# Optimization experiments

Measured on AMD Instinct MI355X. Metric: run time of the kernel, lower is better.

Reference implementation:

```python
import jax, jax.numpy as jnp
import numpy as np
from jax import lax

B, C, TX, TY = 16, 192, 512, 2048
SEG = 8192 // 256  # segment_frames = 32 (hop length 256)
NEG_INF = -1e9


def setup_inputs() -> dict:
    key = jax.random.key(0)
    ks = jax.random.split(key, 7)
    z = jax.random.normal(ks[0], (B, C, TY), jnp.float32)
    z_p = jax.random.normal(ks[1], (B, C, TY), jnp.float32)
    m_p = jax.random.normal(ks[2], (B, C, TX), jnp.float32)
    logs_p = 0.1 * jax.random.normal(ks[3], (B, C, TX), jnp.float32)
    x_lengths = jax.random.randint(ks[4], (B,), TX // 2, TX + 1, jnp.int32)
    y_lengths = jax.random.randint(ks[5], (B,), TY // 2, TY + 1, jnp.int32)
    rand_u = jax.random.uniform(ks[6], (B,), jnp.float32)
    return dict(z=z, z_p=z_p, m_p=m_p, logs_p=logs_p,
                x_lengths=x_lengths, y_lengths=y_lengths, rand_u=rand_u)


def neg_cent_fn(z_p, m_p, logs_p):
    # sum_c -0.5 * exp(-2 logs)[c,tx] * (z_p[c,ty] - m_p[c,tx])^2 - sum_c logs[c,tx]
    # expanded (z-m)^2 = z^2 - 2 z m + m^2 -> batched GEMMs (same math as broadcast form)
    s = jnp.exp(-2.0 * logs_p)                                 # [B,C,Tx]
    a = jnp.einsum('bct,bcs->bts', -0.5 * z_p * z_p, s)        # [B,Ty,Tx]
    b = jnp.einsum('bct,bcs->bts', z_p, s * m_p)               # [B,Ty,Tx]
    c = jnp.sum(-0.5 * s * m_p * m_p - logs_p, axis=1)         # [B,Tx]
    return a + b + c[:, None, :]


def maximum_path_single(value, t_x, t_y):
    # Monotonic alignment search DP on value [Ty,Tx], valid region [:t_y,:t_x].
    Ty, Tx = value.shape
    tx = jnp.arange(Tx)

    def fwd(v, row):
        v_shift = jnp.concatenate([jnp.full((1,), NEG_INF, v.dtype), v[:-1]])
        dirn = v_shift > v                      # True: best predecessor is tx-1
        v_new = row + jnp.maximum(v, v_shift)
        v_new = jnp.where(tx < t_x, v_new, NEG_INF)
        v_new = jnp.maximum(v_new, NEG_INF)     # clamp accumulation
        return v_new, dirn

    v0 = jnp.where(tx == 0, 0.0, NEG_INF)
    _, dirs = lax.scan(fwd, v0, value)          # dirs [Ty,Tx] bool

    def bwd(idx, j):
        active = j < t_y
        idx = jnp.where(j == t_y - 1, t_x - 1, idx)
        row = jnp.where(active, jnp.zeros((Tx,), value.dtype).at[idx].set(1.0), 0.0)
        idx = jnp.where(active, idx - dirs[j, idx].astype(idx.dtype), idx)
        return idx, row

    _, path_rev = lax.scan(bwd, jnp.int32(0), jnp.arange(Ty - 1, -1, -1))
    return path_rev[::-1]                       # [Ty,Tx] 0/1 path


def rand_slice_segments(z, y_lengths, rand_u):
    t = z.shape[2]
    safe = jnp.minimum(y_lengths, t)
    ids_max = jnp.maximum(safe - SEG, 0)
    ids = (rand_u * (ids_max.astype(jnp.float32) + 1e-8)).astype(jnp.int32)
    zs = jax.vmap(lambda zi, s: lax.dynamic_slice_in_dim(zi, s, SEG, axis=1))(z, ids)
    valid = (jnp.arange(SEG)[None, None, :] < (safe - ids)[:, None, None])
    return zs * valid.astype(z.dtype), ids


def reference(z, z_p, m_p, logs_p, x_lengths, y_lengths, rand_u):
    neg_cent = neg_cent_fn(z_p, m_p, logs_p)                     # [B,Ty,Tx]
    attn = jax.vmap(maximum_path_single)(neg_cent, x_lengths, y_lengths)
    attn = lax.stop_gradient(attn)                               # torch: no_grad + detach
    m_p_a = jnp.einsum('bts,bcs->bct', attn, m_p)                # [B,C,Ty]
    logs_p_a = jnp.einsum('bts,bcs->bct', attn, logs_p)          # [B,C,Ty]
    z_slice, ids_slice = rand_slice_segments(z, y_lengths, rand_u)
    return z_slice, ids_slice, attn, m_p_a, logs_p_a
```

## Files before the change

kernel.cpp:

```cpp
#include <hip/hip_runtime.h>
#include <stdint.h>

#define B_   16
#define C_   192
#define TX_  512
#define TY_  2048
#define K_   384
#define SEG_ 32
#define NEG_INF_ (-1e9f)


__global__ __launch_bounds__(128) void k_prep(const float* __restrict__ mp,
                                              const float* __restrict__ logsp,
                                              float* __restrict__ Bmat,
                                              float* __restrict__ cterm) {
    int b  = blockIdx.y;
    int tx = blockIdx.x * 128 + threadIdx.x;
    const float* mb = mp    + (size_t)b * C_ * TX_ + tx;
    const float* lb = logsp + (size_t)b * C_ * TX_ + tx;
    float* B0 = Bmat + (size_t)b * K_ * TX_ + tx;
    float acc = 0.f;
    for (int c = 0; c < C_; ++c) {
        float lg = lb[(size_t)c * TX_];
        float m  = mb[(size_t)c * TX_];
        float s  = expf(-2.f * lg);
        B0[(size_t)c * TX_]        = s;
        B0[(size_t)(C_ + c) * TX_] = s * m;
        acc += -0.5f * s * m * m - lg;
    }
    cterm[b * TX_ + tx] = acc;
}

__global__ __launch_bounds__(256) void k_gemm(const float* __restrict__ zp,
                                              const float* __restrict__ Bmat,
                                              const float* __restrict__ cterm,
                                              float* __restrict__ ncout) {
    __shared__ float As[16][128];
    __shared__ float Bs[16][128];
    int b  = blockIdx.z;
    int m0 = blockIdx.y * 128;
    int n0 = blockIdx.x * 128;
    int tid = threadIdx.x;
    int tm = tid >> 4;
    int tn = tid & 15;
    const float* zpb = zp   + (size_t)b * C_ * TY_;
    const float* Bb  = Bmat + (size_t)b * K_ * TX_;

    float acc[8][8];
#pragma unroll
    for (int i = 0; i < 8; ++i)
#pragma unroll
        for (int j = 0; j < 8; ++j) acc[i][j] = 0.f;

    int lrow = tid >> 5;
    int lcol = (tid & 31) << 2;

    for (int k0 = 0; k0 < K_; k0 += 16) {
        int ksrc = (k0 < C_) ? k0 : (k0 - C_);
        const float* Ab = zpb + (size_t)(ksrc + lrow) * TY_ + m0 + lcol;
        float4 z0 = *(const float4*)Ab;
        float4 z1 = *(const float4*)(Ab + (size_t)8 * TY_);
        if (k0 < C_) {
            z0.x = -0.5f * z0.x * z0.x; z0.y = -0.5f * z0.y * z0.y;
            z0.z = -0.5f * z0.z * z0.z; z0.w = -0.5f * z0.w * z0.w;
            z1.x = -0.5f * z1.x * z1.x; z1.y = -0.5f * z1.y * z1.y;
            z1.z = -0.5f * z1.z * z1.z; z1.w = -0.5f * z1.w * z1.w;
        }
        const float* Bp = Bb + (size_t)(k0 + lrow) * TX_ + n0 + lcol;
        float4 w0 = *(const float4*)Bp;
        float4 w1 = *(const float4*)(Bp + (size_t)8 * TX_);

        __syncthreads();
        *(float4*)&As[lrow][lcol]     = z0;
        *(float4*)&As[lrow + 8][lcol] = z1;
        *(float4*)&Bs[lrow][lcol]     = w0;
        *(float4*)&Bs[lrow + 8][lcol] = w1;
        __syncthreads();

#pragma unroll
        for (int kk = 0; kk < 16; ++kk) {
            float4 a0 = *(const float4*)&As[kk][tm * 8];
            float4 a1 = *(const float4*)&As[kk][tm * 8 + 4];
            float4 b0 = *(const float4*)&Bs[kk][tn * 8];
            float4 b1 = *(const float4*)&Bs[kk][tn * 8 + 4];
            float a[8]  = {a0.x, a0.y, a0.z, a0.w, a1.x, a1.y, a1.z, a1.w};
            float bb[8] = {b0.x, b0.y, b0.z, b0.w, b1.x, b1.y, b1.z, b1.w};
#pragma unroll
            for (int i = 0; i < 8; ++i)
#pragma unroll
                for (int j = 0; j < 8; ++j)
                    acc[i][j] = fmaf(a[i], bb[j], acc[i][j]);
        }
    }

    float cadd[8];
#pragma unroll
    for (int j = 0; j < 8; ++j) cadd[j] = cterm[b * TX_ + n0 + tn * 8 + j];

#pragma unroll
    for (int i = 0; i < 8; ++i) {
        int row = m0 + tm * 8 + i;
        float* orow = ncout + ((size_t)b * TY_ + row) * TX_ + n0 + tn * 8;
        float4 o0, o1;
        o0.x = acc[i][0] + cadd[0]; o0.y = acc[i][1] + cadd[1];
        o0.z = acc[i][2] + cadd[2]; o0.w = acc[i][3] + cadd[3];
        o1.x = acc[i][4] + cadd[4]; o1.y = acc[i][5] + cadd[5];
        o1.z = acc[i][6] + cadd[6]; o1.w = acc[i][7] + cadd[7];
        *(float4*)orow       = o0;
        *(float4*)(orow + 4) = o1;
    }
}

#define NSLOT_ 3

__global__ __launch_bounds__(256, 1) void k_dp(const float* __restrict__ nc,
                                               const int* __restrict__ xl,
                                               const int* __restrict__ yl,
                                               int* __restrict__ path) {
    extern __shared__ unsigned char sdirs[];
    unsigned* sdirs32 = (unsigned*)sdirs;
    float*    stagef  = (float*)(sdirs + 131072);
    unsigned* flags   = (unsigned*)(sdirs + 131072 + NSLOT_ * 8192);
    unsigned* cons_ctr = flags + NSLOT_;

    int b    = blockIdx.x;
    int tid  = threadIdx.x;
    int w    = tid >> 6;
    int lane = tid & 63;
    int t_x  = xl[b];
    int t_y  = yl[b]; if (t_y > TY_) t_y = TY_;
    const float* ncb = nc + (size_t)b * TY_ * TX_;
    int ng = (t_y + 3) >> 2;

    if (tid < NSLOT_ + 1) flags[tid] = 0;
    __syncthreads();

    if (w != 0) {
        int cv = (int)__hip_atomic_load(cons_ctr, __ATOMIC_ACQUIRE,
                                        __HIP_MEMORY_SCOPE_WORKGROUP);
        for (int g = w - 1; g < ng; g += 3) {
            while (cv < g - 2) {
                __builtin_amdgcn_s_sleep(1);
                cv = (int)__hip_atomic_load(cons_ctr, __ATOMIC_ACQUIRE,
                                            __HIP_MEMORY_SCOPE_WORKGROUP);
            }
            int j0 = g * 4;
            float* sb = stagef + (g % NSLOT_) * 2048;
#pragma unroll
            for (int r = 0; r < 4; ++r) {
                const float4* row = (const float4*)(ncb + (size_t)(j0 + r) * TX_);
                float4 q0 = row[2 * lane];
                float4 q1 = row[2 * lane + 1];
                *(float4*)(sb + r * 512 + lane * 4)       = q0;
                *(float4*)(sb + r * 512 + 256 + lane * 4) = q1;
            }
            if (lane == 0)
                __hip_atomic_store(&flags[g % NSLOT_], (unsigned)(g + 1),
                                   __ATOMIC_RELEASE, __HIP_MEMORY_SCOPE_WORKGROUP);
            cv = (int)__hip_atomic_load(cons_ctr, __ATOMIC_ACQUIRE,
                                        __HIP_MEMORY_SCOPE_WORKGROUP);
        }
        return;
    }

    int col0 = lane * 8;
    float v[8];
#pragma unroll
    for (int k = 0; k < 8; ++k) v[k] = (col0 + k == 0) ? 0.f : NEG_INF_;

    const unsigned neg_bits = __float_as_uint(NEG_INF_);
    unsigned fv = 0;
    for (int g = 0; g < ng; ++g) {
        while (fv != (unsigned)(g + 1))
            fv = __hip_atomic_load(&flags[g % NSLOT_], __ATOMIC_ACQUIRE,
                                   __HIP_MEMORY_SCOPE_WORKGROUP);
        unsigned fnx = __hip_atomic_load(&flags[(g + 1) % NSLOT_], __ATOMIC_ACQUIRE,
                                         __HIP_MEMORY_SCOPE_WORKGROUP);
        const float* rowp = stagef + (g % NSLOT_) * 2048;
        unsigned dw = 0u;
#pragma unroll
        for (int r = 0; r < 4; ++r) {
            float4 p0 = *(const float4*)(rowp + r * 512 + lane * 4);
            float4 p1 = *(const float4*)(rowp + r * 512 + 256 + lane * 4);
            float rc[8] = {p0.x, p0.y, p0.z, p0.w, p1.x, p1.y, p1.z, p1.w};
            float left = __uint_as_float(__builtin_amdgcn_update_dpp(
                (int)neg_bits, (int)__float_as_uint(v[7]),
                0x138 , 0xF, 0xF, false));
            unsigned by = 0u;
#pragma unroll
            for (int k = 7; k >= 0; --k) {
                float vs = (k == 0) ? left : v[k - 1];
                if (vs > v[k]) by |= (1u << k);
                v[k] = fmaxf(v[k], vs) + rc[k];
            }
            dw |= by << (8 * r);
        }
        sdirs32[g * 64 + lane] = dw;
        if (lane == 0)
            __hip_atomic_store(cons_ctr, (unsigned)(g + 1),
                               __ATOMIC_RELEASE, __HIP_MEMORY_SCOPE_WORKGROUP);
        fv = fnx;
    }

    int* pb = path + b * TY_;
    for (int j = t_y + lane; j < TY_; j += 64) pb[j] = -1;

    if (lane == 0) {
        int idx = t_x - 1;
        int j   = t_y - 1;
        while (j >= 0) {
            int n  = (j + 1 < 8) ? (j + 1) : 8;
            int bs = (idx - 7) >> 3; if (bs < 0) bs = 0;
            int b2 = bs + 1;         if (b2 > 63) b2 = 63;
            unsigned lo[8], hi[8];
#pragma unroll
            for (int r = 0; r < 8; ++r) {
                if (r < n) {
                    int jr = j - r;
                    int rb = (jr >> 2) * 256 + (jr & 3);
                    lo[r] = sdirs[rb + bs * 4];
                    hi[r] = sdirs[rb + b2 * 4];
                }
            }
#pragma unroll
            for (int r = 0; r < 8; ++r) {
                if (r < n) {
                    pb[j - r] = idx;
                    int Bi = idx >> 3;
                    unsigned byte = (Bi == bs) ? lo[r] : hi[r];
                    idx -= (int)((byte >> (idx & 7)) & 1u);
                }
            }
            j -= n;
        }
    }
}

__global__ __launch_bounds__(256) void k_attn(const int* __restrict__ path,
                                              float* __restrict__ attn) {
    int i   = blockIdx.x * 256 + threadIdx.x;
    int tx0 = (i & 127) << 2;
    int bty = i >> 7;
    int p   = path[bty];
    float4 o;
    o.x = (p == tx0)     ? 1.f : 0.f;
    o.y = (p == tx0 + 1) ? 1.f : 0.f;
    o.z = (p == tx0 + 2) ? 1.f : 0.f;
    o.w = (p == tx0 + 3) ? 1.f : 0.f;
    ((float4*)attn)[i] = o;
}

__global__ __launch_bounds__(256) void k_proj(const int* __restrict__ path,
                                              const float* __restrict__ mp,
                                              const float* __restrict__ logsp,
                                              float* __restrict__ mpa,
                                              float* __restrict__ logsa) {
    int i   = blockIdx.x * 256 + threadIdx.x;
    int ty0 = (i & 511) << 2;
    int bc  = i >> 9;
    int b   = bc / C_;
    const int4 p4 = *(const int4*)(path + b * TY_ + ty0);
    const float* mrow = mp    + (size_t)bc * TX_;
    const float* lrow = logsp + (size_t)bc * TX_;
    float4 mo, lo;
    mo.x = (p4.x >= 0) ? mrow[p4.x] : 0.f;  lo.x = (p4.x >= 0) ? lrow[p4.x] : 0.f;
    mo.y = (p4.y >= 0) ? mrow[p4.y] : 0.f;  lo.y = (p4.y >= 0) ? lrow[p4.y] : 0.f;
    mo.z = (p4.z >= 0) ? mrow[p4.z] : 0.f;  lo.z = (p4.z >= 0) ? lrow[p4.z] : 0.f;
    mo.w = (p4.w >= 0) ? mrow[p4.w] : 0.f;  lo.w = (p4.w >= 0) ? lrow[p4.w] : 0.f;
    ((float4*)mpa)[i]   = mo;
    ((float4*)logsa)[i] = lo;
}

__global__ __launch_bounds__(256) void k_slice(const float* __restrict__ z,
                                               const int* __restrict__ yl,
                                               const float* __restrict__ ru,
                                               float* __restrict__ zs,
                                               float* __restrict__ oid) {
    int b = blockIdx.x;
    int safe = yl[b]; if (safe > TY_) safe = TY_;
    int idsmax = safe - SEG_; if (idsmax < 0) idsmax = 0;
    int ids = (int)(ru[b] * ((float)idsmax + 1e-8f));
    int lim = safe - ids;
    for (int t = threadIdx.x; t < C_ * SEG_; t += 256) {
        int c = t >> 5, k = t & 31;
        zs[b * C_ * SEG_ + t] =
            (k < lim) ? z[((size_t)b * C_ + c) * TY_ + ids + k] : 0.f;
    }
    if (threadIdx.x == 0) oid[b] = (float)ids;
}

extern "C" void kernel_launch(void* const* d_in, const int* in_sizes, int n_in,
                              void* d_out, int out_size, void* d_ws, size_t ws_size,
                              hipStream_t stream) {
    const float* z     = (const float*)d_in[0];
    const float* zp    = (const float*)d_in[1];
    const float* mp    = (const float*)d_in[2];
    const float* logsp = (const float*)d_in[3];
    const int*   xl    = (const int*)d_in[4];
    const int*   yl    = (const int*)d_in[5];
    const float* ru    = (const float*)d_in[6];

    float* out     = (float*)d_out;
    float* o_zs    = out;
    float* o_ids   = out + 98304;
    float* o_attn  = out + 98320;
    float* o_mpa   = out + 16875536;
    float* o_logsa = out + 23166992;

    float* Bmat  = (float*)d_ws;
    float* cterm = Bmat + (size_t)B_ * K_ * TX_;
    int*   path  = (int*)(cterm + B_ * TX_);

    const int dp_lds = 131072 + NSLOT_ * 8192 + 64;

    hipFuncSetAttribute((const void*)k_dp,
                        hipFuncAttributeMaxDynamicSharedMemorySize, dp_lds);

    hipLaunchKernelGGL(k_prep, dim3(TX_ / 128, B_), dim3(128), 0, stream,
                       mp, logsp, Bmat, cterm);
    hipLaunchKernelGGL(k_gemm, dim3(TX_ / 128, TY_ / 128, B_), dim3(256), 0, stream,
                       zp, Bmat, cterm, o_attn);
    hipLaunchKernelGGL(k_dp, dim3(B_), dim3(256), dp_lds, stream,
                       o_attn, xl, yl, path);
    hipLaunchKernelGGL(k_attn, dim3(B_ * TY_ * TX_ / 4 / 256), dim3(256), 0, stream,
                       path, o_attn);
    hipLaunchKernelGGL(k_proj, dim3(B_ * C_ * TY_ / 4 / 256), dim3(256), 0, stream,
                       path, mp, logsp, o_mpa, o_logsa);
    hipLaunchKernelGGL(k_slice, dim3(B_), dim3(256), 0, stream,
                       z, yl, ru, o_zs, o_ids);
}
```

Measured before the change: 843.4 us.

## Deepen DP producer pipeline and spill direction bits to global memory

The DP kernel now runs 512 threads with 7 producer waves and a 14-slot LDS staging ring, where before it had 3 producers and 3 slots. The goal is to keep the serial forward wavefront from stalling on loads of neg_cent rows. To free LDS for the larger ring, direction bytes go to a global workspace instead of LDS. The backtrack now stages 64-row windows cooperatively from global into LDS before lane 0 walks them. This adds global write and read traffic and a waitcnt fence, and relies on workspace space that was not allocated before.

```diff
diff --git a/kernel.cpp b/kernel.cpp
--- a/kernel.cpp
+++ b/kernel.cpp
@@ -111,17 +111,18 @@
     }
 }
 
-#define NSLOT_ 3
-
-__global__ __launch_bounds__(256, 1) void k_dp(const float* __restrict__ nc,
+#define NS_ 14
+#define NP_ 7
+
+__global__ __launch_bounds__(512, 1) void k_dp(const float* __restrict__ nc,
                                                const int* __restrict__ xl,
                                                const int* __restrict__ yl,
-                                               int* __restrict__ path) {
-    extern __shared__ unsigned char sdirs[];
-    unsigned* sdirs32 = (unsigned*)sdirs;
-    float*    stagef  = (float*)(sdirs + 131072);
-    unsigned* flags   = (unsigned*)(sdirs + 131072 + NSLOT_ * 8192);
-    unsigned* cons_ctr = flags + NSLOT_;
+                                               int* __restrict__ path,
+                                               unsigned char* __restrict__ gdirs) {
+    extern __shared__ unsigned char slds[];
+    float*    stagef   = (float*)slds;
+    unsigned* flags    = (unsigned*)(slds + NS_ * 8192);
+    unsigned* cons_ctr = flags + NS_;
 
     int b    = blockIdx.x;
     int tid  = threadIdx.x;
@@ -130,22 +131,23 @@
     int t_x  = xl[b];
     int t_y  = yl[b]; if (t_y > TY_) t_y = TY_;
     const float* ncb = nc + (size_t)b * TY_ * TX_;
+    unsigned char* gb = gdirs + (size_t)b * (TY_ * 64);
     int ng = (t_y + 3) >> 2;
 
-    if (tid < NSLOT_ + 1) flags[tid] = 0;
+    if (tid < NS_ + 1) flags[tid] = 0u;
     __syncthreads();
 
     if (w != 0) {
         int cv = (int)__hip_atomic_load(cons_ctr, __ATOMIC_ACQUIRE,
                                         __HIP_MEMORY_SCOPE_WORKGROUP);
-        for (int g = w - 1; g < ng; g += 3) {
-            while (cv < g - 2) {
+        for (int g = w - 1; g < ng; g += NP_) {
+            while (cv < g - (NS_ - 1)) {
                 __builtin_amdgcn_s_sleep(1);
                 cv = (int)__hip_atomic_load(cons_ctr, __ATOMIC_ACQUIRE,
                                             __HIP_MEMORY_SCOPE_WORKGROUP);
             }
             int j0 = g * 4;
-            float* sb = stagef + (g % NSLOT_) * 2048;
+            float* sb = stagef + (g % NS_) * 2048;
 #pragma unroll
             for (int r = 0; r < 4; ++r) {
                 const float4* row = (const float4*)(ncb + (size_t)(j0 + r) * TX_);
@@ -155,7 +157,7 @@
                 *(float4*)(sb + r * 512 + 256 + lane * 4) = q1;
             }
             if (lane == 0)
-                __hip_atomic_store(&flags[g % NSLOT_], (unsigned)(g + 1),
+                __hip_atomic_store(&flags[g % NS_], (unsigned)(g + 1),
                                    __ATOMIC_RELEASE, __HIP_MEMORY_SCOPE_WORKGROUP);
             cv = (int)__hip_atomic_load(cons_ctr, __ATOMIC_ACQUIRE,
                                         __HIP_MEMORY_SCOPE_WORKGROUP);
@@ -172,11 +174,11 @@
     unsigned fv = 0;
     for (int g = 0; g < ng; ++g) {
         while (fv != (unsigned)(g + 1))
-            fv = __hip_atomic_load(&flags[g % NSLOT_], __ATOMIC_ACQUIRE,
+            fv = __hip_atomic_load(&flags[g % NS_], __ATOMIC_ACQUIRE,
                                    __HIP_MEMORY_SCOPE_WORKGROUP);
-        unsigned fnx = __hip_atomic_load(&flags[(g + 1) % NSLOT_], __ATOMIC_ACQUIRE,
+        unsigned fnx = __hip_atomic_load(&flags[(g + 1) % NS_], __ATOMIC_ACQUIRE,
                                          __HIP_MEMORY_SCOPE_WORKGROUP);
-        const float* rowp = stagef + (g % NSLOT_) * 2048;
+        const float* rowp = stagef + (g % NS_) * 2048;
         unsigned dw = 0u;
 #pragma unroll
         for (int r = 0; r < 4; ++r) {
@@ -195,44 +197,59 @@
             }
             dw |= by << (8 * r);
         }
-        sdirs32[g * 64 + lane] = dw;
+        int j0 = g * 4;
+        gb[(size_t)(j0    ) * 64 + lane] = (unsigned char)(dw      );
+        gb[(size_t)(j0 + 1) * 64 + lane] = (unsigned char)(dw >>  8);
+        gb[(size_t)(j0 + 2) * 64 + lane] = (unsigned char)(dw >> 16);
+        gb[(size_t)(j0 + 3) * 64 + lane] = (unsigned char)(dw >> 24);
         if (lane == 0)
             __hip_atomic_store(cons_ctr, (unsigned)(g + 1),
                                __ATOMIC_RELEASE, __HIP_MEMORY_SCOPE_WORKGROUP);
         fv = fnx;
     }
 
+    __builtin_amdgcn_s_waitcnt(3952);
+
     int* pb = path + b * TY_;
-    for (int j = t_y + lane; j < TY_; j += 64) pb[j] = -1;
-
-    if (lane == 0) {
-        int idx = t_x - 1;
-        int j   = t_y - 1;
-        while (j >= 0) {
-            int n  = (j + 1 < 8) ? (j + 1) : 8;
-            int bs = (idx - 7) >> 3; if (bs < 0) bs = 0;
-            int b2 = bs + 1;         if (b2 > 63) b2 = 63;
-            unsigned lo[8], hi[8];
-#pragma unroll
-            for (int r = 0; r < 8; ++r) {
-                if (r < n) {
-                    int jr = j - r;
-                    int rb = (jr >> 2) * 256 + (jr & 3);
-                    lo[r] = sdirs[rb + bs * 4];
-                    hi[r] = sdirs[rb + b2 * 4];
+    for (int j2 = t_y + lane; j2 < TY_; j2 += 64) pb[j2] = -1;
+
+    unsigned char* swin = (unsigned char*)stagef;
+    int j   = t_y - 1;
+    int idx = t_x - 1;
+    while (j >= 0) {
+        int nb = (j + 1 < 64) ? (j + 1) : 64;
+        if (lane < nb) {
+            const uint4* rp = (const uint4*)(gb + (size_t)(j - lane) * 64);
+            uint4 a0 = rp[0], a1 = rp[1], a2 = rp[2], a3 = rp[3];
+            uint4* wp = (uint4*)(swin + lane * 64);
+            wp[0] = a0; wp[1] = a1; wp[2] = a2; wp[3] = a3;
+        }
+        if (lane == 0) {
+            int r2 = 0;
+            while (r2 < nb) {
+                int n = nb - r2; if (n > 8) n = 8;
+                int Bhi = idx >> 3;
+                int Blo = Bhi - 1; if (Blo < 0) Blo = 0;
+                unsigned lo8[8], hi8[8];
+#pragma unroll
+                for (int r = 0; r < 8; ++r) {
+                    if (r < n) {
+                        lo8[r] = swin[(r2 + r) * 64 + Blo];
+                        hi8[r] = swin[(r2 + r) * 64 + Bhi];
+                    }
                 }
+#pragma unroll
+                for (int r = 0; r < 8; ++r) {
+                    if (r < n) {
+                        pb[j - (r2 + r)] = idx;
+                        unsigned byte = ((idx >> 3) == Bhi) ? hi8[r] : lo8[r];
+                        idx -= (int)((byte >> (idx & 7)) & 1u);
+                    }
+                }
+                r2 += n;
             }
-#pragma unroll
-            for (int r = 0; r < 8; ++r) {
-                if (r < n) {
-                    pb[j - r] = idx;
-                    int Bi = idx >> 3;
-                    unsigned byte = (Bi == bs) ? lo[r] : hi[r];
-                    idx -= (int)((byte >> (idx & 7)) & 1u);
-                }
-            }
-            j -= n;
-        }
+        }
+        j -= nb;
     }
 }
 
@@ -307,11 +324,12 @@
     float* o_mpa   = out + 16875536;
     float* o_logsa = out + 23166992;
 
-    float* Bmat  = (float*)d_ws;
-    float* cterm = Bmat + (size_t)B_ * K_ * TX_;
-    int*   path  = (int*)(cterm + B_ * TX_);
-
-    const int dp_lds = 131072 + NSLOT_ * 8192 + 64;
+    float*         Bmat  = (float*)d_ws;
+    float*         cterm = Bmat + (size_t)B_ * K_ * TX_;
+    int*           path  = (int*)(cterm + B_ * TX_);
+    unsigned char* gdirs = (unsigned char*)(path + B_ * TY_);
+
+    const int dp_lds = NS_ * 8192 + 64;
 
     hipFuncSetAttribute((const void*)k_dp,
                         hipFuncAttributeMaxDynamicSharedMemorySize, dp_lds);
@@ -320,8 +338,8 @@
                        mp, logsp, Bmat, cterm);
     hipLaunchKernelGGL(k_gemm, dim3(TX_ / 128, TY_ / 128, B_), dim3(256), 0, stream,
                        zp, Bmat, cterm, o_attn);
-    hipLaunchKernelGGL(k_dp, dim3(B_), dim3(256), dp_lds, stream,
-                       o_attn, xl, yl, path);
+    hipLaunchKernelGGL(k_dp, dim3(B_), dim3(512), dp_lds, stream,
+                       o_attn, xl, yl, path, gdirs);
     hipLaunchKernelGGL(k_attn, dim3(B_ * TY_ * TX_ / 4 / 256), dim3(256), 0, stream,
                        path, o_attn);
     hipLaunchKernelGGL(k_proj, dim3(B_ * C_ * TY_ / 4 / 256), dim3(256), 0, stream,
```

Measured after the change: 781.7 us. 7.3% less time.
